# Kernel optimization log

Measured on AMD Instinct MI355X. Metric: run time of the kernel, lower is better.

The kernel has to match this reference:

```python
import jax, jax.numpy as jnp
import numpy as np

N_QUBITS = 7
N_LAYERS = 2
DIM = 2 ** N_QUBITS  # 128
NORM_FACTOR = 1.0


def _cnot_gather_idx(n):
    # CNOT chain (0,1),(1,2),...,(n-2,n-1) plus wraparound (n-1,0).
    # new_state[x] = old_state[idx[x]]; apply gates in reverse to arange.
    gates = [(i, i + 1) for i in range(n - 1)] + [(n - 1, 0)]
    idx = np.arange(2 ** n)
    for c, t in reversed(gates):
        cbit = 1 << (n - 1 - c)  # pennylane wire 0 = most significant bit
        tbit = 1 << (n - 1 - t)
        idx = np.where((idx & cbit) > 0, idx ^ tbit, idx)
    return jnp.asarray(idx)

CNOT_IDX = _cnot_gather_idx(N_QUBITS)


def silu(x):
    return x * jax.nn.sigmoid(x)


def cayley(A_real, A_imag):
    # Hermitianize then Cayley transform -> unitary, per layer. [L,D,D]
    A = A_real.astype(jnp.complex64) + 1j * A_imag.astype(jnp.complex64)
    A = A + jnp.conj(jnp.swapaxes(A, -1, -2))
    I = jnp.eye(DIM, dtype=A.dtype)
    return jnp.matmul(A - 1j * I, jnp.linalg.inv(A + 1j * I))


def _single_qubit_gate(theta_x, theta_y):
    # combined G = RY(theta_y) @ RX(theta_x) applied to every qubit
    cx, sx = jnp.cos(theta_x / 2), jnp.sin(theta_x / 2)
    cy, sy = jnp.cos(theta_y / 2), jnp.sin(theta_y / 2)
    RX = jnp.stack([jnp.stack([cx + 0j, -1j * sx]), jnp.stack([-1j * sx, cx + 0j])])
    RY = jnp.stack([jnp.stack([cy + 0j, -sy + 0j]), jnp.stack([sy + 0j, cy + 0j])])
    return RY @ RX


def quantum_evolve(psi, coeffs, q_mats):
    # psi: [N, DIM] complex64 normalized state vectors
    N = psi.shape[0]
    for j in range(N_LAYERS):
        psi = psi @ q_mats[j].T  # QubitUnitary: new = U @ old
        G = _single_qubit_gate(coeffs[j, 0], coeffs[j, 1])
        psi = psi.reshape((N,) + (2,) * N_QUBITS)
        for ax in range(1, N_QUBITS + 1):
            psi = jnp.moveaxis(jnp.tensordot(G, psi, axes=((1,), (ax,))), 0, ax)
        psi = psi.reshape(N, DIM)
        psi = psi[:, CNOT_IDX]  # CNOT chain is a fixed basis permutation
    return psi


def setup_inputs() -> dict:
    key = jax.random.key(0)
    ks = jax.random.split(key, 16)
    N, E = 50000, 800000
    in_nf, hid, out_nf = 128, 128, 128
    h = jax.random.normal(ks[0], (N, in_nf), dtype=jnp.float32)
    edge_index = jax.random.randint(ks[1], (2, E), 0, N)
    s = 0.05
    W_e1 = jax.random.normal(ks[2], (2 * in_nf, hid), dtype=jnp.float32) * s
    b_e1 = jnp.zeros((hid,), dtype=jnp.float32)
    W_e2 = jax.random.normal(ks[3], (hid, hid), dtype=jnp.float32) * s
    b_e2 = jnp.zeros((hid,), dtype=jnp.float32)
    W_enc = jax.random.normal(ks[4], (hid + in_nf, DIM), dtype=jnp.float32) * s
    b_enc = jnp.zeros((DIM,), dtype=jnp.float32)
    coeffs = jax.random.normal(ks[5], (N_LAYERS, 2), dtype=jnp.float32) * 0.1
    A_real = jax.random.normal(ks[6], (N_LAYERS, DIM, DIM), dtype=jnp.float32) * 0.01
    A_imag = jax.random.normal(ks[7], (N_LAYERS, DIM, DIM), dtype=jnp.float32) * 0.01
    W_dec = jax.random.normal(ks[8], (DIM, out_nf), dtype=jnp.float32) * s
    b_dec = jnp.zeros((out_nf,), dtype=jnp.float32)
    return {"h": h, "edge_index": edge_index, "W_e1": W_e1, "b_e1": b_e1,
            "W_e2": W_e2, "b_e2": b_e2, "W_enc": W_enc, "b_enc": b_enc,
            "coeffs": coeffs, "A_real": A_real, "A_imag": A_imag,
            "W_dec": W_dec, "b_dec": b_dec}


def reference(h, edge_index, W_e1, b_e1, W_e2, b_e2, W_enc, b_enc,
              coeffs, A_real, A_imag, W_dec, b_dec):
    row, col = edge_index[0], edge_index[1]
    # edge model: mij = MLP([h_src, h_tgt])
    e = jnp.concatenate([h[row], h[col]], axis=1)  # [E, 2*in_nf]
    e = silu(e @ W_e1 + b_e1)
    edge_feat = silu(e @ W_e2 + b_e2)  # [E, hid]
    # node model: scatter-sum aggregation over destination `row`
    agg = jax.ops.segment_sum(edge_feat, row, num_segments=h.shape[0]) / NORM_FACTOR
    q_input = jnp.concatenate([h, agg], axis=1) @ W_enc + b_enc  # [N, DIM]
    norm = jnp.sqrt(jnp.sum(q_input ** 2, axis=1, keepdims=True) + 1e-12)
    psi = (q_input / norm).astype(jnp.complex64)
    q_mats = cayley(A_real, A_imag)  # [L, DIM, DIM] unitary
    psi = quantum_evolve(psi, coeffs, q_mats)
    out = h + (jnp.real(psi) @ W_dec + b_dec)
    return out, edge_feat
```

## Files before the change

### kernel.cpp

```cpp
#include <hip/hip_runtime.h>
#include <math.h>

#define N_NODES 50000
#define N_EDGES 800000

#define EDGE_MAIN_BLOCKS 224
#define MAIN_TILES 198
#define MAIN_TOTAL (EDGE_MAIN_BLOCKS * MAIN_TILES)
#define DC_TOTAL (N_EDGES / 16 - MAIN_TOTAL)

typedef __attribute__((ext_vector_type(8))) short bf16x8;
typedef __attribute__((ext_vector_type(4))) short bf16x4;
typedef __attribute__((ext_vector_type(2))) short shortx2;
typedef __attribute__((ext_vector_type(4))) float f32x4;

__device__ __forceinline__ float silu_f(float x) {
    float d = 1.0f + __expf(-x);
    return x * __builtin_amdgcn_rcpf(d);
}

__device__ __forceinline__ unsigned short f2bf(float x) {
    union { float f; unsigned u; } v; v.f = x;
    unsigned r = v.u + 0x7FFFu + ((v.u >> 16) & 1u);
    return (unsigned short)(r >> 16);
}

__device__ __forceinline__ void atomic_pk_add_bf16(short* addr, shortx2 v) {
    typedef shortx2 __attribute__((address_space(1)))* gp1;
    __builtin_amdgcn_global_atomic_fadd_v2bf16((gp1)(unsigned long long)addr, v);
}

__device__ __forceinline__ void dbar(int* ctr, int target) {
    __threadfence();
    __syncthreads();
    if (threadIdx.x == 0) {
        __hip_atomic_fetch_add(ctr, 1, __ATOMIC_RELEASE, __HIP_MEMORY_SCOPE_AGENT);
        while (__hip_atomic_load(ctr, __ATOMIC_RELAXED, __HIP_MEMORY_SCOPE_AGENT) < target) {
            __builtin_amdgcn_s_sleep(2);
        }
    }
    __syncthreads();
    __threadfence();
}

__global__ __launch_bounds__(256) void prep_kernel(const float* __restrict__ h,
                                                   short* __restrict__ hbf,
                                                   const int* __restrict__ ei,
                                                   int* __restrict__ cnt,
                                                   const float* __restrict__ A_real,
                                                   const float* __restrict__ A_imag,
                                                   float* __restrict__ H,
                                                   float* __restrict__ X) {
    const int bid = blockIdx.x;
    const int t = threadIdx.x;
    if (bid < 3125) {
        int i = bid * 256 + t;
        const float4* h4 = (const float4*)h;
        float4 v0 = h4[i * 2], v1 = h4[i * 2 + 1];
        bf16x8 b;
        b[0] = (short)f2bf(v0.x); b[1] = (short)f2bf(v0.y);
        b[2] = (short)f2bf(v0.z); b[3] = (short)f2bf(v0.w);
        b[4] = (short)f2bf(v1.x); b[5] = (short)f2bf(v1.y);
        b[6] = (short)f2bf(v1.z); b[7] = (short)f2bf(v1.w);
        ((bf16x8*)hbf)[i] = b;
        atomicAdd(&cnt[ei[i]], 1);
    } else {
        int p = bid - 3125;
        int L = p >> 2, q4 = p & 3;
        const float* ar = A_real + L * 16384;
        const float* ai = A_imag + L * 16384;
        float* hre = H + L * 32768;
        float* him = hre + 16384;
        float* xre = X + L * 32768;
        float* xim = xre + 16384;
        for (int m = 0; m < 16; ++m) {
            int idx = q4 * 4096 + t + 256 * m;
            int i = idx >> 7, j = idx & 127;
            float hr = ar[idx] + ar[j * 128 + i];
            float hi = ai[idx] - ai[j * 128 + i];
            hre[idx] = hr;
            him[idx] = hi;
            xre[idx] = hr;
            xim[idx] = hi - (i == j ? 1.0f : 0.0f);
        }
    }
}

__device__ __forceinline__ void ns_t_body(int blk, int t,
                                          const float* __restrict__ H,
                                          const float* __restrict__ X,
                                          float* __restrict__ T) {
    const int L = blk >> 4;
    const int i = (blk & 15) * 8 + (t >> 7);
    const int j = t & 127;
    const float* hre = H + L * 32768;
    const float* him = hre + 16384;
    const float* xre = X + L * 32768;
    const float* xim = xre + 16384;
    float accr = 0.f, acci = 0.f;
    #pragma unroll 4
    for (int k = 0; k < 128; ++k) {
        float hr = hre[i * 128 + k], hi = him[i * 128 + k];
        float xr = xre[k * 128 + j], xi = xim[k * 128 + j];
        accr += hr * xr - hi * xi;
        acci += hr * xi + hi * xr;
    }
    T[L * 32768 + i * 128 + j]          = accr - xim[i * 128 + j];
    T[L * 32768 + 16384 + i * 128 + j]  = acci + xre[i * 128 + j];
}

__device__ __forceinline__ void ns_x_body(int blk, int t,
                                          const float* __restrict__ X,
                                          const float* __restrict__ T,
                                          float* __restrict__ Xout) {
    const int L = blk >> 4;
    const int i = (blk & 15) * 8 + (t >> 7);
    const int j = t & 127;
    const float* xre = X + L * 32768;
    const float* xim = xre + 16384;
    const float* tre = T + L * 32768;
    const float* tim = tre + 16384;
    float accr = 0.f, acci = 0.f;
    #pragma unroll 4
    for (int k = 0; k < 128; ++k) {
        float xr = xre[i * 128 + k], xi = xim[i * 128 + k];
        float tr = tre[k * 128 + j], ti = tim[k * 128 + j];
        accr += xr * tr - xi * ti;
        acci += xr * ti + xi * tr;
    }
    Xout[L * 32768 + i * 128 + j]          = 2.0f * xre[i * 128 + j] - accr;
    Xout[L * 32768 + 16384 + i * 128 + j]  = 2.0f * xim[i * 128 + j] - acci;
}

__global__ __launch_bounds__(1024) void nst_scan_kernel(const float* __restrict__ H,
                                                        const float* __restrict__ X,
                                                        float* __restrict__ T,
                                                        const int* __restrict__ cnt,
                                                        int* __restrict__ cursor) {
    const int bid = blockIdx.x;
    const int t = threadIdx.x;
    if (bid < 32) { ns_t_body(bid, t, H, X, T); return; }
    __shared__ int sA[1024];
    __shared__ int sB[1024];
    const int CH = 49;
    int s = 0;
    #pragma unroll 4
    for (int i = 0; i < CH; ++i) {
        int idx = t * CH + i;
        if (idx < N_NODES) s += cnt[idx];
    }
    sA[t] = s;
    __syncthreads();
    int* src = sA;
    int* dst = sB;
    for (int off = 1; off < 1024; off <<= 1) {
        int v = src[t];
        if (t >= off) v += src[t - off];
        dst[t] = v;
        __syncthreads();
        int* tmp = src; src = dst; dst = tmp;
    }
    int run = (t == 0) ? 0 : src[t - 1];
    for (int i = 0; i < CH; ++i) {
        int idx = t * CH + i;
        if (idx < N_NODES) {
            cursor[idx] = run;
            run += cnt[idx];
        }
    }
}

__global__ __launch_bounds__(1024) void fill_nsx_kernel(const int* __restrict__ ei,
                                                        int* __restrict__ cursor,
                                                        int* __restrict__ elist,
                                                        const float* __restrict__ X,
                                                        const float* __restrict__ T,
                                                        float* __restrict__ Xout) {
    const int bid = blockIdx.x;
    const int t = threadIdx.x;
    if (bid < 782) {
        int e = bid * 1024 + t;
        if (e < N_EDGES) {
            int slot = atomicAdd(&cursor[ei[e]], 1);
            elist[slot] = e;
        }
        return;
    }
    ns_x_body(bid - 782, t, X, T, Xout);
}

__global__ __launch_bounds__(768)
__attribute__((amdgpu_waves_per_eu(3, 3)))
void edge_dchain_kernel(const short* __restrict__ hbf,
                        const int* __restrict__ ei,
                        const int* __restrict__ elist,
                        const float* __restrict__ W_e1,
                        const float* __restrict__ b_e1,
                        const float* __restrict__ W_e2,
                        const float* __restrict__ b_e2,
                        float* __restrict__ ef_out,
                        short* __restrict__ agg_bf,
                        const float* __restrict__ H,
                        const float* __restrict__ Xb,
                        float* __restrict__ T,
                        float* __restrict__ Xa,
                        const float* __restrict__ coeffs,
                        float* __restrict__ Y,
                        float* __restrict__ ReM,
                        const float* __restrict__ W_dec,
                        short* __restrict__ Dt,
                        int* __restrict__ ctr) {
    __shared__ __align__(16) char smraw[133120];
    short* w1f = (short*)smraw;
    short* w2f = (short*)(smraw + 65536);
    short* c1s = (short*)(smraw + 98304);
    float* smf = (float*)smraw;

    const int bid = blockIdx.x;
    const int t = threadIdx.x;
    const int lane = t & 63;
    const int w = t >> 6;
    const int l15 = lane & 15;
    const int kg = lane >> 4;

    int tstart, tstop;
    if (bid < EDGE_MAIN_BLOCKS) {
        tstart = bid * MAIN_TILES;
        tstop  = tstart + MAIN_TILES;
    } else {
        const int db = bid - EDGE_MAIN_BLOCKS;
        for (int idx = t; idx < 1024; idx += 768) ns_t_body(db, idx, H, Xb, T);
        dbar(ctr + 0, 32);
        for (int idx = t; idx < 1024; idx += 768) ns_x_body(db, idx, Xb, T, Xa);
        dbar(ctr + 1, 32);
        if (db < 2) {
            float* Mre = smf;
            float* Mim = smf + 128 * 129;
            const float* xre = Xa + db * 32768;
            const float* xim = xre + 16384;
            for (int idx = t; idx < 16384; idx += 768) {
                int i = idx >> 7, j = idx & 127;
                Mre[i * 129 + j] = (i == j ? 1.0f : 0.0f) + 2.0f * xim[idx];
                Mim[i * 129 + j] = -2.0f * xre[idx];
            }
            __syncthreads();
            const float tx = coeffs[2 * db + 0] * 0.5f;
            const float ty = coeffs[2 * db + 1] * 0.5f;
            const float cx = cosf(tx), sx = sinf(tx), cy = cosf(ty), sy = sinf(ty);
            const float G00r = cx * cy, G00i = sx * sy;
            const float G01r = -cx * sy, G01i = -sx * cy;
            const float G10r = cx * sy, G10i = -sx * cy;
            const float G11r = cx * cy, G11i = -sx * sy;
            for (int st = 0; st < 7; ++st) {
                int b = 1 << st;
                for (int pid = t; pid < 8192; pid += 768) {
                    int col = pid & 127, ph = pid >> 7;
                    int i0 = ((ph >> st) << (st + 1)) | (ph & (b - 1));
                    int i1 = i0 | b;
                    float v0r = Mre[i0 * 129 + col], v0i = Mim[i0 * 129 + col];
                    float v1r = Mre[i1 * 129 + col], v1i = Mim[i1 * 129 + col];
                    Mre[i0 * 129 + col] = G00r * v0r - G00i * v0i + G01r * v1r - G01i * v1i;
                    Mim[i0 * 129 + col] = G00r * v0i + G00i * v0r + G01r * v1i + G01i * v1r;
                    Mre[i1 * 129 + col] = G10r * v0r - G10i * v0i + G11r * v1r - G11i * v1i;
                    Mim[i1 * 129 + col] = G10r * v0i + G10i * v0r + G11r * v1i + G11i * v1r;
                }
                __syncthreads();
            }
            const int cs[7] = {6, 5, 4, 3, 2, 1, 0};
            const int ts[7] = {0, 6, 5, 4, 3, 2, 1};
            float* yre = Y + db * 32768;
            float* yim = yre + 16384;
            for (int idx = t; idx < 16384; idx += 768) {
                int ii_ = idx >> 7, col = idx & 127;
                int s = ii_;
                #pragma unroll
                for (int m = 0; m < 7; ++m) {
                    int cbit = 1 << (6 - cs[m]);
                    int tbit = 1 << (6 - ts[m]);
                    if (s & cbit) s ^= tbit;
                }
                yre[idx] = Mre[s * 129 + col];
                yim[idx] = Mim[s * 129 + col];
            }
        }
        dbar(ctr + 2, 32);
        {
            float* q1r = smf;
            float* q1i = smf + 16384;
            for (int idx = t; idx < 16384; idx += 768) {
                q1r[idx] = Y[idx];
                q1i[idx] = Y[16384 + idx];
            }
            __syncthreads();
            if (t < 512) {
                int o = db * 512 + t;
                int i = o >> 7, j = o & 127;
                const float* q2re = Y + 32768;
                const float* q2im = Y + 49152;
                float acc = 0.f;
                for (int k = 0; k < 128; ++k) {
                    acc += q2re[i * 128 + k] * q1r[k * 128 + j]
                         - q2im[i * 128 + k] * q1i[k * 128 + j];
                }
                ReM[o] = acc;
            }
        }
        dbar(ctr + 3, 32);
        {
            float* ml = smf;
            float* wl = smf + 16384;
            for (int idx = t; idx < 16384; idx += 768) {
                ml[idx] = ReM[idx];
                wl[idx] = W_dec[idx];
            }
            __syncthreads();
            if (t < 512) {
                int o = db * 512 + t;
                int k = o >> 7, j = o & 127;
                float acc = 0.f;
                for (int i = 0; i < 128; ++i) {
                    acc += ml[i * 128 + k] * wl[i * 128 + j];
                }
                Dt[j * 128 + k] = (short)f2bf(acc);
            }
            __syncthreads();
        }
        tstart = MAIN_TOTAL + (DC_TOTAL * db) / 32;
        tstop  = MAIN_TOTAL + (DC_TOTAL * (db + 1)) / 32;
    }

    {
        const float4* w1_4 = (const float4*)W_e1;
        for (int idx4 = t; idx4 < 8192; idx4 += 768) {
            int k = idx4 >> 5, j4 = idx4 & 31;
            float4 v = w1_4[idx4];
            int s = k >> 5, kgs = (k >> 3) & 3, e = k & 7;
            int fb = s * 8;
            float vz[4] = {v.x, v.y, v.z, v.w};
            #pragma unroll
            for (int z = 0; z < 4; ++z) {
                int j = j4 * 4 + z;
                int nf = j >> 4, jl = j & 15;
                w1f[((fb + nf) * 64 + kgs * 16 + jl) * 8 + e] = (short)f2bf(vz[z]);
            }
        }
        const float4* w2_4 = (const float4*)W_e2;
        for (int idx4 = t; idx4 < 4096; idx4 += 768) {
            int k = idx4 >> 5, j4 = idx4 & 31;
            float4 v = w2_4[idx4];
            int s2 = k >> 5, kgs = (k >> 3) & 3, e = k & 7;
            int fb = s2 * 8;
            float vz[4] = {v.x, v.y, v.z, v.w};
            #pragma unroll
            for (int z = 0; z < 4; ++z) {
                int j = j4 * 4 + z;
                int nf = j >> 4, jl = j & 15;
                w2f[((fb + nf) * 64 + kgs * 16 + jl) * 8 + e] = (short)f2bf(vz[z]);
            }
        }
    }
    float b1v[8], b2v[8];
    #pragma unroll
    for (int nf = 0; nf < 8; ++nf) {
        b1v[nf] = b_e1[nf * 16 + l15];
        b2v[nf] = b_e2[nf * 16 + l15];
    }
    __syncthreads();

    const bf16x8* hb8 = (const bf16x8*)hbf;
    const bf16x8* w1v = (const bf16x8*)w1f;
    const bf16x8* w2v = (const bf16x8*)w2f;
    short* myc1 = &c1s[w * 1088];
    const int span = tstop - tstart;
    int tile = tstart + (span * w) / 12;
    const int tend = tstart + (span * (w + 1)) / 12;
    if (tile >= tend) return;

    int el = elist[tile * 16 + l15];
    int ri = ei[el];
    int ci = ei[N_EDGES + el];
    bf16x8 a1[8];
    #pragma unroll
    for (int s = 0; s < 4; ++s) a1[s] = hb8[(size_t)ri * 16 + s * 4 + kg];
    #pragma unroll
    for (int s = 0; s < 4; ++s) a1[4 + s] = hb8[(size_t)ci * 16 + s * 4 + kg];

    bool hn = (tile + 1 < tend);
    int eln = 0, rin = 0, cin = 0;
    if (hn) {
        eln = elist[(tile + 1) * 16 + l15];
        rin = ei[eln];
        cin = ei[N_EDGES + eln];
    }

    float runsum[8];
    #pragma unroll
    for (int nf = 0; nf < 8; ++nf) runsum[nf] = 0.f;

    for (;;) {
        bool hn2 = (tile + 2 < tend);
        int eln2 = 0, rin2 = 0, cin2 = 0;
        if (hn2) {
            eln2 = elist[(tile + 2) * 16 + l15];
            rin2 = ei[eln2];
            cin2 = ei[N_EDGES + eln2];
        }

        f32x4 acc[8];
        #pragma unroll
        for (int nf = 0; nf < 8; ++nf) acc[nf] = (f32x4){0.f, 0.f, 0.f, 0.f};
        __builtin_amdgcn_s_setprio(1);
        #pragma unroll
        for (int s = 0; s < 8; ++s) {
            #pragma unroll
            for (int nf = 0; nf < 8; ++nf) {
                bf16x8 b = w1v[(s * 8 + nf) * 64 + lane];
                acc[nf] = __builtin_amdgcn_mfma_f32_16x16x32_bf16(a1[s], b, acc[nf], 0, 0, 0);
            }
        }
        __builtin_amdgcn_s_setprio(0);

        bf16x8 a1n[8];
        if (hn) {
            #pragma unroll
            for (int s = 0; s < 4; ++s) a1n[s] = hb8[(size_t)rin * 16 + s * 4 + kg];
            #pragma unroll
            for (int s = 0; s < 4; ++s) a1n[4 + s] = hb8[(size_t)cin * 16 + s * 4 + kg];
        }

        f32x4 acc2[8];
        #pragma unroll
        for (int nf = 0; nf < 8; ++nf) acc2[nf] = (f32x4){0.f, 0.f, 0.f, 0.f};
        #pragma unroll
        for (int half = 0; half < 2; ++half) {
            #pragma unroll
            for (int nfh = 0; nfh < 4; ++nfh) {
                int nf = half * 4 + nfh;
                #pragma unroll
                for (int r = 0; r < 4; ++r) {
                    int row = kg * 4 + r;
                    int c = nfh * 16 + l15;
                    myc1[row * 68 + c] = (short)f2bf(silu_f(acc[nf][r] + b1v[nf]));
                }
            }
            #pragma unroll
            for (int s2l = 0; s2l < 2; ++s2l) {
                int k0h = s2l * 32 + kg * 8;
                int base = l15 * 68 + k0h;
                bf16x4 lo = *(const bf16x4*)&myc1[base];
                bf16x4 hi = *(const bf16x4*)&myc1[base + 4];
                bf16x8 a2;
                #pragma unroll
                for (int z = 0; z < 4; ++z) { a2[z] = lo[z]; a2[4 + z] = hi[z]; }
                int s2 = half * 2 + s2l;
                __builtin_amdgcn_s_setprio(1);
                #pragma unroll
                for (int nf = 0; nf < 8; ++nf) {
                    bf16x8 b = w2v[(s2 * 8 + nf) * 64 + lane];
                    acc2[nf] = __builtin_amdgcn_mfma_f32_16x16x32_bf16(a2, b, acc2[nf], 0, 0, 0);
                }
                __builtin_amdgcn_s_setprio(0);
            }
        }

        int rw[4], ew[4];
        #pragma unroll
        for (int r = 0; r < 4; ++r) {
            rw[r] = __shfl(ri, kg * 4 + r);
            ew[r] = __shfl(el, kg * 4 + r);
        }
        int rwn0 = hn ? __shfl(rin, kg * 4) : -1;
        #pragma unroll
        for (int r = 0; r < 4; ++r) {
            float* efp = ef_out + (size_t)ew[r] * 128;
            #pragma unroll
            for (int nf = 0; nf < 8; ++nf) {
                int col = nf * 16 + l15;
                float v = silu_f(acc2[nf][r] + b2v[nf]);
                __builtin_nontemporal_store(v, efp + col);
                runsum[nf] += v;
            }
            bool end = (r < 3) ? (rw[r + 1] != rw[r]) : (rw[3] != rwn0);
            if (end) {
                short* agp = agg_bf + (size_t)rw[r] * 128;
                #pragma unroll
                for (int nf = 0; nf < 8; ++nf) {
                    float vn = __shfl_xor(runsum[nf], 1);
                    if ((l15 & 1) == 0) {
                        shortx2 pk;
                        pk.x = (short)f2bf(runsum[nf]);
                        pk.y = (short)f2bf(vn);
                        atomic_pk_add_bf16(agp + nf * 16 + l15, pk);
                    }
                    runsum[nf] = 0.f;
                }
            }
        }

        if (!hn) break;
        tile += 1;
        el = eln; ri = rin; ci = cin;
        #pragma unroll
        for (int s = 0; s < 8; ++s) a1[s] = a1n[s];
        hn = hn2; eln = eln2; rin = rin2; cin = cin2;
    }
}

__global__ __launch_bounds__(1024)
__attribute__((amdgpu_waves_per_eu(4, 4)))
void node_kernel(const short* __restrict__ hbf,
                 const short* __restrict__ agg_bf,
                 const float* __restrict__ W_enc,
                 const float* __restrict__ b_enc,
                 const short* __restrict__ Dt_bf,
                 const float* __restrict__ b_dec,
                 const float* __restrict__ h,
                 float* __restrict__ out) {
    __shared__ short wef[64 * 64 * 8];
    __shared__ short dtf[32 * 64 * 8];
    __shared__ short c1s[16][16 * 68];

    const int t = threadIdx.x;
    const int lane = t & 63;
    const int w = t >> 6;
    const int l15 = lane & 15;
    const int kg = lane >> 4;

    {
        const float4* we4 = (const float4*)W_enc;
        for (int idx4 = t; idx4 < 8192; idx4 += 1024) {
            int k = idx4 >> 5, j4 = idx4 & 31;
            float4 v = we4[idx4];
            int s = k >> 5, kgs = (k >> 3) & 3, e = k & 7;
            int fb = s * 8;
            float vz[4] = {v.x, v.y, v.z, v.w};
            #pragma unroll
            for (int z = 0; z < 4; ++z) {
                int j = j4 * 4 + z;
                int nf = j >> 4, jl = j & 15;
                wef[((fb + nf) * 64 + kgs * 16 + jl) * 8 + e] = (short)f2bf(vz[z]);
            }
        }
        const bf16x8* dt8 = (const bf16x8*)Dt_bf;
        bf16x8* dtv = (bf16x8*)dtf;
        for (int idx8 = t; idx8 < 2048; idx8 += 1024) {
            int brow = idx8 >> 4, kslot = idx8 & 15;
            int s2 = kslot >> 2, kgs = kslot & 3;
            int nf = brow >> 4, jl = brow & 15;
            dtv[(s2 * 8 + nf) * 64 + kgs * 16 + jl] = dt8[idx8];
        }
    }
    float bj1[8], bj2[8];
    #pragma unroll
    for (int nf = 0; nf < 8; ++nf) {
        bj1[nf] = b_enc[nf * 16 + l15];
        bj2[nf] = b_dec[nf * 16 + l15];
    }
    __syncthreads();

    const bf16x8* hb8 = (const bf16x8*)hbf;
    const bf16x8* ab8 = (const bf16x8*)agg_bf;
    const bf16x8* wev = (const bf16x8*)wef;
    const bf16x8* dtv = (const bf16x8*)dtf;
    short* myc1 = &c1s[w][0];
    const int nt = N_NODES / 16;
    const int tile = blockIdx.x * 16 + w;
    if (tile >= nt) return;

    const int node = tile * 16 + l15;
    bf16x8 a[8];
    #pragma unroll
    for (int s = 0; s < 4; ++s) a[s] = hb8[(size_t)node * 16 + s * 4 + kg];
    #pragma unroll
    for (int s = 0; s < 4; ++s) a[4 + s] = ab8[(size_t)node * 16 + s * 4 + kg];

    f32x4 acc[8];
    #pragma unroll
    for (int nf = 0; nf < 8; ++nf) acc[nf] = (f32x4){0.f, 0.f, 0.f, 0.f};
    __builtin_amdgcn_s_setprio(1);
    #pragma unroll
    for (int s = 0; s < 8; ++s) {
        #pragma unroll
        for (int nf = 0; nf < 8; ++nf) {
            bf16x8 b = wev[(s * 8 + nf) * 64 + lane];
            acc[nf] = __builtin_amdgcn_mfma_f32_16x16x32_bf16(a[s], b, acc[nf], 0, 0, 0);
        }
    }
    __builtin_amdgcn_s_setprio(0);

    float nr[4] = {0.f, 0.f, 0.f, 0.f};
    #pragma unroll
    for (int nf = 0; nf < 8; ++nf) {
        #pragma unroll
        for (int r = 0; r < 4; ++r) {
            acc[nf][r] += bj1[nf];
            nr[r] += acc[nf][r] * acc[nf][r];
        }
    }
    #pragma unroll
    for (int r = 0; r < 4; ++r) {
        nr[r] += __shfl_xor(nr[r], 1);
        nr[r] += __shfl_xor(nr[r], 2);
        nr[r] += __shfl_xor(nr[r], 4);
        nr[r] += __shfl_xor(nr[r], 8);
        nr[r] = 1.0f / sqrtf(nr[r] + 1e-12f);
    }

    f32x4 acc2[8];
    #pragma unroll
    for (int nf = 0; nf < 8; ++nf) acc2[nf] = (f32x4){0.f, 0.f, 0.f, 0.f};
    #pragma unroll
    for (int half = 0; half < 2; ++half) {
        #pragma unroll
        for (int nfh = 0; nfh < 4; ++nfh) {
            int nf = half * 4 + nfh;
            #pragma unroll
            for (int r = 0; r < 4; ++r) {
                int row = kg * 4 + r;
                int c = nfh * 16 + l15;
                myc1[row * 68 + c] = (short)f2bf(acc[nf][r] * nr[r]);
            }
        }
        #pragma unroll
        for (int s2l = 0; s2l < 2; ++s2l) {
            int k0h = s2l * 32 + kg * 8;
            int base = l15 * 68 + k0h;
            bf16x4 lo = *(const bf16x4*)&myc1[base];
            bf16x4 hi = *(const bf16x4*)&myc1[base + 4];
            bf16x8 a2;
            #pragma unroll
            for (int z = 0; z < 4; ++z) { a2[z] = lo[z]; a2[4 + z] = hi[z]; }
            int s2 = half * 2 + s2l;
            __builtin_amdgcn_s_setprio(1);
            #pragma unroll
            for (int nf = 0; nf < 8; ++nf) {
                bf16x8 b = dtv[(s2 * 8 + nf) * 64 + lane];
                acc2[nf] = __builtin_amdgcn_mfma_f32_16x16x32_bf16(a2, b, acc2[nf], 0, 0, 0);
            }
            __builtin_amdgcn_s_setprio(0);
        }
    }

    #pragma unroll
    for (int r = 0; r < 4; ++r) {
        size_t rowb = (size_t)(tile * 16 + kg * 4 + r) * 128;
        #pragma unroll
        for (int nf = 0; nf < 8; ++nf) {
            int col = nf * 16 + l15;
            out[rowb + col] = h[rowb + col] + acc2[nf][r] + bj2[nf];
        }
    }
}

extern "C" void kernel_launch(void* const* d_in, const int* in_sizes, int n_in,
                              void* d_out, int out_size, void* d_ws, size_t ws_size,
                              hipStream_t stream) {
    const float* h      = (const float*)d_in[0];
    const int*   ei     = (const int*)d_in[1];
    const float* W_e1   = (const float*)d_in[2];
    const float* b_e1   = (const float*)d_in[3];
    const float* W_e2   = (const float*)d_in[4];
    const float* b_e2   = (const float*)d_in[5];
    const float* W_enc  = (const float*)d_in[6];
    const float* b_enc  = (const float*)d_in[7];
    const float* coeffs = (const float*)d_in[8];
    const float* A_real = (const float*)d_in[9];
    const float* A_imag = (const float*)d_in[10];
    const float* W_dec  = (const float*)d_in[11];
    const float* b_dec  = (const float*)d_in[12];

    float* out    = (float*)d_out;
    float* ef_out = out + (size_t)N_NODES * 128;

    short* agg_bf = (short*)d_ws;
    int*   cnt    = (int*)(agg_bf + (size_t)N_NODES * 128);
    int*   ctr    = cnt + 50176;
    short* h_bf   = (short*)(ctr + 16);
    int*   cursor = (int*)(h_bf + (size_t)N_NODES * 128);
    int*   elist  = cursor + 50176;
    float* small  = (float*)(elist + N_EDGES);
    float* Ybuf   = small;
    float* ReM    = Ybuf + 65536;
    float* Hbuf   = ReM + 16384;
    float* Xa     = Hbuf + 65536;
    float* Xb     = Xa + 65536;
    float* Tbuf   = Xb + 65536;
    short* Dt_bf  = (short*)(Tbuf + 65536);

    hipMemsetAsync(agg_bf, 0,
                   (size_t)N_NODES * 128 * sizeof(short) + 50176 * sizeof(int) + 64,
                   stream);

    prep_kernel<<<3133, 256, 0, stream>>>(h, h_bf, ei, cnt, A_real, A_imag, Hbuf, Xa);
    nst_scan_kernel<<<33, 1024, 0, stream>>>(Hbuf, Xa, Tbuf, cnt, cursor);
    fill_nsx_kernel<<<814, 1024, 0, stream>>>(ei, cursor, elist, Xa, Tbuf, Xb);

    edge_dchain_kernel<<<256, 768, 0, stream>>>(h_bf, ei, elist, W_e1, b_e1, W_e2, b_e2,
                                                ef_out, agg_bf,
                                                Hbuf, Xb, Tbuf, Xa, coeffs, Ybuf, ReM,
                                                W_dec, Dt_bf, ctr);

    node_kernel<<<196, 1024, 0, stream>>>(h_bf, agg_bf, W_enc, b_enc, Dt_bf, b_dec, h, out);
}
```

Measured before the change: 711.0 us.

## Split decoder-chain work out of edge kernel into a separate serial kernel

Moves the Cayley/Newton-Schulz tail, gate application and decoder matrix products out of the fused edge kernel into their own 32-block kernel launched before the edge kernel. The edge kernel now spreads all edge tiles evenly across all 256 blocks instead of giving the last 32 blocks extra chain work plus fewer tiles. This removes the imbalance and the grid-barrier coupling inside the edge kernel. In exchange the chain work no longer overlaps with edge processing and runs serially before it.

```diff
diff --git a/kernel.cpp b/kernel.cpp
--- a/kernel.cpp
+++ b/kernel.cpp
@@ -3,11 +3,6 @@
 
 #define N_NODES 50000
 #define N_EDGES 800000
-
-#define EDGE_MAIN_BLOCKS 224
-#define MAIN_TILES 198
-#define MAIN_TOTAL (EDGE_MAIN_BLOCKS * MAIN_TILES)
-#define DC_TOTAL (N_EDGES / 16 - MAIN_TOTAL)
 
 typedef __attribute__((ext_vector_type(8))) short bf16x8;
 typedef __attribute__((ext_vector_type(4))) short bf16x4;
@@ -189,145 +184,150 @@
     ns_x_body(bid - 782, t, X, T, Xout);
 }
 
+__global__ __launch_bounds__(1024) void dtail_kernel(const float* __restrict__ H,
+                                                     const float* __restrict__ Xb,
+                                                     float* __restrict__ T,
+                                                     float* __restrict__ Xa,
+                                                     const float* __restrict__ coeffs,
+                                                     float* __restrict__ Y,
+                                                     float* __restrict__ ReM,
+                                                     const float* __restrict__ W_dec,
+                                                     short* __restrict__ Dt,
+                                                     int* __restrict__ ctr) {
+    __shared__ float smem[128 * 129 * 2];
+    const int bid = blockIdx.x;
+    const int t = threadIdx.x;
+
+    ns_t_body(bid, t, H, Xb, T);
+    dbar(ctr + 0, 32);
+    ns_x_body(bid, t, Xb, T, Xa);
+    dbar(ctr + 1, 32);
+
+    if (bid < 2) {
+        float* Mre = smem;
+        float* Mim = smem + 128 * 129;
+        const int L = bid;
+        const float* xre = Xa + L * 32768;
+        const float* xim = xre + 16384;
+        for (int q = 0; q < 16; ++q) {
+            int idx = t + 1024 * q;
+            int i = idx >> 7, j = idx & 127;
+            Mre[i * 129 + j] = (i == j ? 1.0f : 0.0f) + 2.0f * xim[idx];
+            Mim[i * 129 + j] = -2.0f * xre[idx];
+        }
+        __syncthreads();
+
+        const float tx = coeffs[2 * L + 0] * 0.5f;
+        const float ty = coeffs[2 * L + 1] * 0.5f;
+        const float cx = cosf(tx), sx = sinf(tx), cy = cosf(ty), sy = sinf(ty);
+        const float G00r = cx * cy, G00i = sx * sy;
+        const float G01r = -cx * sy, G01i = -sx * cy;
+        const float G10r = cx * sy, G10i = -sx * cy;
+        const float G11r = cx * cy, G11i = -sx * sy;
+
+        for (int st = 0; st < 7; ++st) {
+            int b = 1 << st;
+            #pragma unroll
+            for (int p = 0; p < 8; ++p) {
+                int pid = t + 1024 * p;
+                int col = pid & 127, ph = pid >> 7;
+                int i0 = ((ph >> st) << (st + 1)) | (ph & (b - 1));
+                int i1 = i0 | b;
+                float v0r = Mre[i0 * 129 + col], v0i = Mim[i0 * 129 + col];
+                float v1r = Mre[i1 * 129 + col], v1i = Mim[i1 * 129 + col];
+                Mre[i0 * 129 + col] = G00r * v0r - G00i * v0i + G01r * v1r - G01i * v1i;
+                Mim[i0 * 129 + col] = G00r * v0i + G00i * v0r + G01r * v1i + G01i * v1r;
+                Mre[i1 * 129 + col] = G10r * v0r - G10i * v0i + G11r * v1r - G11i * v1i;
+                Mim[i1 * 129 + col] = G10r * v0i + G10i * v0r + G11r * v1i + G11i * v1r;
+            }
+            __syncthreads();
+        }
+
+        const int cs[7] = {6, 5, 4, 3, 2, 1, 0};
+        const int ts[7] = {0, 6, 5, 4, 3, 2, 1};
+        float* yre = Y + L * 32768;
+        float* yim = yre + 16384;
+        for (int q = 0; q < 16; ++q) {
+            int idx = t + 1024 * q;
+            int ii_ = idx >> 7, col = idx & 127;
+            int s = ii_;
+            #pragma unroll
+            for (int m = 0; m < 7; ++m) {
+                int cbit = 1 << (6 - cs[m]);
+                int tbit = 1 << (6 - ts[m]);
+                if (s & cbit) s ^= tbit;
+            }
+            yre[idx] = Mre[s * 129 + col];
+            yim[idx] = Mim[s * 129 + col];
+        }
+    }
+    dbar(ctr + 2, 32);
+
+    {
+        float* q1r = smem;
+        float* q1i = smem + 16384;
+        __syncthreads();
+        for (int idx = t; idx < 16384; idx += 1024) {
+            q1r[idx] = Y[idx];
+            q1i[idx] = Y[16384 + idx];
+        }
+        __syncthreads();
+        if (t < 512) {
+            int o = bid * 512 + t;
+            int i = o >> 7, j = o & 127;
+            const float* q2re = Y + 32768;
+            const float* q2im = Y + 49152;
+            float acc = 0.f;
+            for (int k = 0; k < 128; ++k) {
+                acc += q2re[i * 128 + k] * q1r[k * 128 + j]
+                     - q2im[i * 128 + k] * q1i[k * 128 + j];
+            }
+            ReM[o] = acc;
+        }
+    }
+    dbar(ctr + 3, 32);
+
+    {
+        float* ml = smem;
+        float* wl = smem + 16384;
+        __syncthreads();
+        for (int idx = t; idx < 16384; idx += 1024) {
+            ml[idx] = ReM[idx];
+            wl[idx] = W_dec[idx];
+        }
+        __syncthreads();
+        if (t < 512) {
+            int o = bid * 512 + t;
+            int k = o >> 7, j = o & 127;
+            float acc = 0.f;
+            for (int i = 0; i < 128; ++i) {
+                acc += ml[i * 128 + k] * wl[i * 128 + j];
+            }
+            Dt[j * 128 + k] = (short)f2bf(acc);
+        }
+    }
+}
+
 __global__ __launch_bounds__(768)
 __attribute__((amdgpu_waves_per_eu(3, 3)))
-void edge_dchain_kernel(const short* __restrict__ hbf,
-                        const int* __restrict__ ei,
-                        const int* __restrict__ elist,
-                        const float* __restrict__ W_e1,
-                        const float* __restrict__ b_e1,
-                        const float* __restrict__ W_e2,
-                        const float* __restrict__ b_e2,
-                        float* __restrict__ ef_out,
-                        short* __restrict__ agg_bf,
-                        const float* __restrict__ H,
-                        const float* __restrict__ Xb,
-                        float* __restrict__ T,
-                        float* __restrict__ Xa,
-                        const float* __restrict__ coeffs,
-                        float* __restrict__ Y,
-                        float* __restrict__ ReM,
-                        const float* __restrict__ W_dec,
-                        short* __restrict__ Dt,
-                        int* __restrict__ ctr) {
-    __shared__ __align__(16) char smraw[133120];
-    short* w1f = (short*)smraw;
-    short* w2f = (short*)(smraw + 65536);
-    short* c1s = (short*)(smraw + 98304);
-    float* smf = (float*)smraw;
-
-    const int bid = blockIdx.x;
+void edge_kernel(const short* __restrict__ hbf,
+                 const int* __restrict__ ei,
+                 const int* __restrict__ elist,
+                 const float* __restrict__ W_e1,
+                 const float* __restrict__ b_e1,
+                 const float* __restrict__ W_e2,
+                 const float* __restrict__ b_e2,
+                 float* __restrict__ ef_out,
+                 short* __restrict__ agg_bf) {
+    __shared__ short w1f[64 * 64 * 8];
+    __shared__ short w2f[32 * 64 * 8];
+    __shared__ short c1s[12][16 * 68];
+
     const int t = threadIdx.x;
     const int lane = t & 63;
     const int w = t >> 6;
     const int l15 = lane & 15;
     const int kg = lane >> 4;
-
-    int tstart, tstop;
-    if (bid < EDGE_MAIN_BLOCKS) {
-        tstart = bid * MAIN_TILES;
-        tstop  = tstart + MAIN_TILES;
-    } else {
-        const int db = bid - EDGE_MAIN_BLOCKS;
-        for (int idx = t; idx < 1024; idx += 768) ns_t_body(db, idx, H, Xb, T);
-        dbar(ctr + 0, 32);
-        for (int idx = t; idx < 1024; idx += 768) ns_x_body(db, idx, Xb, T, Xa);
-        dbar(ctr + 1, 32);
-        if (db < 2) {
-            float* Mre = smf;
-            float* Mim = smf + 128 * 129;
-            const float* xre = Xa + db * 32768;
-            const float* xim = xre + 16384;
-            for (int idx = t; idx < 16384; idx += 768) {
-                int i = idx >> 7, j = idx & 127;
-                Mre[i * 129 + j] = (i == j ? 1.0f : 0.0f) + 2.0f * xim[idx];
-                Mim[i * 129 + j] = -2.0f * xre[idx];
-            }
-            __syncthreads();
-            const float tx = coeffs[2 * db + 0] * 0.5f;
-            const float ty = coeffs[2 * db + 1] * 0.5f;
-            const float cx = cosf(tx), sx = sinf(tx), cy = cosf(ty), sy = sinf(ty);
-            const float G00r = cx * cy, G00i = sx * sy;
-            const float G01r = -cx * sy, G01i = -sx * cy;
-            const float G10r = cx * sy, G10i = -sx * cy;
-            const float G11r = cx * cy, G11i = -sx * sy;
-            for (int st = 0; st < 7; ++st) {
-                int b = 1 << st;
-                for (int pid = t; pid < 8192; pid += 768) {
-                    int col = pid & 127, ph = pid >> 7;
-                    int i0 = ((ph >> st) << (st + 1)) | (ph & (b - 1));
-                    int i1 = i0 | b;
-                    float v0r = Mre[i0 * 129 + col], v0i = Mim[i0 * 129 + col];
-                    float v1r = Mre[i1 * 129 + col], v1i = Mim[i1 * 129 + col];
-                    Mre[i0 * 129 + col] = G00r * v0r - G00i * v0i + G01r * v1r - G01i * v1i;
-                    Mim[i0 * 129 + col] = G00r * v0i + G00i * v0r + G01r * v1i + G01i * v1r;
-                    Mre[i1 * 129 + col] = G10r * v0r - G10i * v0i + G11r * v1r - G11i * v1i;
-                    Mim[i1 * 129 + col] = G10r * v0i + G10i * v0r + G11r * v1i + G11i * v1r;
-                }
-                __syncthreads();
-            }
-            const int cs[7] = {6, 5, 4, 3, 2, 1, 0};
-            const int ts[7] = {0, 6, 5, 4, 3, 2, 1};
-            float* yre = Y + db * 32768;
-            float* yim = yre + 16384;
-            for (int idx = t; idx < 16384; idx += 768) {
-                int ii_ = idx >> 7, col = idx & 127;
-                int s = ii_;
-                #pragma unroll
-                for (int m = 0; m < 7; ++m) {
-                    int cbit = 1 << (6 - cs[m]);
-                    int tbit = 1 << (6 - ts[m]);
-                    if (s & cbit) s ^= tbit;
-                }
-                yre[idx] = Mre[s * 129 + col];
-                yim[idx] = Mim[s * 129 + col];
-            }
-        }
-        dbar(ctr + 2, 32);
-        {
-            float* q1r = smf;
-            float* q1i = smf + 16384;
-            for (int idx = t; idx < 16384; idx += 768) {
-                q1r[idx] = Y[idx];
-                q1i[idx] = Y[16384 + idx];
-            }
-            __syncthreads();
-            if (t < 512) {
-                int o = db * 512 + t;
-                int i = o >> 7, j = o & 127;
-                const float* q2re = Y + 32768;
-                const float* q2im = Y + 49152;
-                float acc = 0.f;
-                for (int k = 0; k < 128; ++k) {
-                    acc += q2re[i * 128 + k] * q1r[k * 128 + j]
-                         - q2im[i * 128 + k] * q1i[k * 128 + j];
-                }
-                ReM[o] = acc;
-            }
-        }
-        dbar(ctr + 3, 32);
-        {
-            float* ml = smf;
-            float* wl = smf + 16384;
-            for (int idx = t; idx < 16384; idx += 768) {
-                ml[idx] = ReM[idx];
-                wl[idx] = W_dec[idx];
-            }
-            __syncthreads();
-            if (t < 512) {
-                int o = db * 512 + t;
-                int k = o >> 7, j = o & 127;
-                float acc = 0.f;
-                for (int i = 0; i < 128; ++i) {
-                    acc += ml[i * 128 + k] * wl[i * 128 + j];
-                }
-                Dt[j * 128 + k] = (short)f2bf(acc);
-            }
-            __syncthreads();
-        }
-        tstart = MAIN_TOTAL + (DC_TOTAL * db) / 32;
-        tstop  = MAIN_TOTAL + (DC_TOTAL * (db + 1)) / 32;
-    }
 
     {
         const float4* w1_4 = (const float4*)W_e1;
@@ -370,10 +370,12 @@
     const bf16x8* hb8 = (const bf16x8*)hbf;
     const bf16x8* w1v = (const bf16x8*)w1f;
     const bf16x8* w2v = (const bf16x8*)w2f;
-    short* myc1 = &c1s[w * 1088];
-    const int span = tstop - tstart;
-    int tile = tstart + (span * w) / 12;
-    const int tend = tstart + (span * (w + 1)) / 12;
+    short* myc1 = &c1s[w][0];
+    const int nt = N_EDGES / 16;
+    const int TW = gridDim.x * 12;
+    const int wvid = blockIdx.x * 12 + w;
+    int tile = (int)(((long long)nt * wvid) / TW);
+    const int tend = (int)(((long long)nt * (wvid + 1)) / TW);
     if (tile >= tend) return;
 
     int el = elist[tile * 16 + l15];
@@ -694,11 +696,11 @@
     prep_kernel<<<3133, 256, 0, stream>>>(h, h_bf, ei, cnt, A_real, A_imag, Hbuf, Xa);
     nst_scan_kernel<<<33, 1024, 0, stream>>>(Hbuf, Xa, Tbuf, cnt, cursor);
     fill_nsx_kernel<<<814, 1024, 0, stream>>>(ei, cursor, elist, Xa, Tbuf, Xb);
-
-    edge_dchain_kernel<<<256, 768, 0, stream>>>(h_bf, ei, elist, W_e1, b_e1, W_e2, b_e2,
-                                                ef_out, agg_bf,
-                                                Hbuf, Xb, Tbuf, Xa, coeffs, Ybuf, ReM,
-                                                W_dec, Dt_bf, ctr);
+    dtail_kernel<<<32, 1024, 0, stream>>>(Hbuf, Xb, Tbuf, Xa, coeffs, Ybuf, ReM,
+                                          W_dec, Dt_bf, ctr);
+
+    edge_kernel<<<256, 768, 0, stream>>>(h_bf, ei, elist, W_e1, b_e1, W_e2, b_e2,
+                                         ef_out, agg_bf);
 
     node_kernel<<<196, 1024, 0, stream>>>(h_bf, agg_bf, W_enc, b_enc, Dt_bf, b_dec, h, out);
 }
```

Result: faster. 663.4 us (-6.7%).
